# Kernel tuning notes

Measured on AMD Instinct MI355X. Metric: run time of the kernel, lower is better.

The kernel has to match this reference:

```python
import jax, jax.numpy as jnp
import numpy as np

B = 4096
HIST = 50
VOCAB = 100000
PAD_IDX = 179
EMB_DIM = 64           # sparse_dim_after_embedding
DENSE = 256            # dense_feature_number
PROJ_IN = 768          # emb_feature_dim_before_project
PROJ_HID = 256
PROJ_OUT = 64          # emb_feature_dim
BOT = (512, 64)        # bottom_mlp_dims
ALL_DIM = EMB_DIM + BOT[1] + PROJ_OUT        # 192
OUT_DIM = ALL_DIM * (ALL_DIM + 1) // 2 + BOT[1]  # 18592
TOP = (1024, 512)      # top_mlp_dims
BN_EPS = 1e-5

# precomputed upper-triangular (incl. diagonal) indices, row-major like torch mask extract
_TRIU_R, _TRIU_C = np.triu_indices(ALL_DIM)


def setup_inputs() -> dict:
    key = jax.random.key(0)
    ks = jax.random.split(key, 20)
    s = 0.02
    emb_table = jax.random.normal(ks[0], (VOCAB, EMB_DIM), jnp.float32) * s
    emb_table = emb_table.at[PAD_IDX].set(0.0)  # padding_idx=179
    return {
        "x_sparse": jax.random.randint(ks[1], (B, HIST), 0, VOCAB),
        "x_dense": jax.random.normal(ks[2], (B, DENSE), jnp.float32),
        "x_embed_before_projection": jax.random.normal(ks[3], (B, PROJ_IN), jnp.float32),
        "emb_table": emb_table,
        "pw1": jax.random.normal(ks[4], (PROJ_IN, PROJ_HID), jnp.float32) * s,
        "pb1": jnp.zeros((PROJ_HID,), jnp.float32),
        "pw2": jax.random.normal(ks[5], (PROJ_HID, PROJ_OUT), jnp.float32) * s,
        "pb2": jnp.zeros((PROJ_OUT,), jnp.float32),
        "bn_gamma": jnp.ones((PROJ_OUT,), jnp.float32),
        "bn_beta": jnp.zeros((PROJ_OUT,), jnp.float32),
        "bw1": jax.random.normal(ks[6], (DENSE, BOT[0]), jnp.float32) * s,
        "bb1": jnp.zeros((BOT[0],), jnp.float32),
        "bw2": jax.random.normal(ks[7], (BOT[0], BOT[1]), jnp.float32) * s,
        "bb2": jnp.zeros((BOT[1],), jnp.float32),
        "tw1": jax.random.normal(ks[8], (OUT_DIM, TOP[0]), jnp.float32) * s,
        "tb1": jnp.zeros((TOP[0],), jnp.float32),
        "tw2": jax.random.normal(ks[9], (TOP[0], TOP[1]), jnp.float32) * s,
        "tb2": jnp.zeros((TOP[1],), jnp.float32),
        "tw3": jax.random.normal(ks[10], (TOP[1], 1), jnp.float32) * s,
        "tb3": jnp.zeros((1,), jnp.float32),
    }


def reference(x_sparse, x_dense, x_embed_before_projection, emb_table,
              pw1, pb1, pw2, pb2, bn_gamma, bn_beta,
              bw1, bb1, bw2, bb2, tw1, tb1, tw2, tb2, tw3, tb3):
    # embedding-sum over history: [B, HIST, EMB_DIM] -> [B, EMB_DIM]
    embed_x = jnp.sum(emb_table[x_sparse], axis=1)

    # ContrastiveNet: Linear -> ReLU -> Linear -> BatchNorm1d (batch stats, training fwd)
    h = jax.nn.relu(x_embed_before_projection @ pw1 + pb1)
    z = h @ pw2 + pb2
    mu = jnp.mean(z, axis=0)
    var = jnp.var(z, axis=0)  # biased variance, as torch BN uses for normalization
    x_embed = bn_gamma * (z - mu) * jax.lax.rsqrt(var + BN_EPS) + bn_beta

    # bottom MLP (dropout = identity at inference)
    bottom = jax.nn.relu(jax.nn.relu(x_dense @ bw1 + bb1) @ bw2 + bb2)

    concat_first = jnp.concatenate([bottom, x_embed, embed_x], axis=-1)  # [B, 192]

    # pairwise dot-product interaction; pack upper triangle incl. diagonal
    dot = jnp.einsum('bi,bj->bij', concat_first, concat_first)  # [B, 192, 192]
    interaction = dot[:, _TRIU_R, _TRIU_C]  # [B, 192*193/2]

    concat_second = jnp.concatenate([interaction, bottom], axis=-1)  # [B, OUT_DIM]

    t = jax.nn.relu(concat_second @ tw1 + tb1)
    t = jax.nn.relu(t @ tw2 + tb2)
    output = jax.nn.sigmoid(t @ tw3 + tb3)  # [B, 1]
    # squeeze(-1).squeeze().unsqueeze(1) -> [B, 1]
    output = output.reshape(-1, 1)
    return output, x_embed
```

## Files before the change

kernel.cpp:

```cpp
#include <hip/hip_runtime.h>
#include <hip/hip_bf16.h>
#include <cstdint>
#include <cstddef>

typedef __bf16 bf16;
typedef unsigned char u8;
typedef unsigned short u16;
typedef __bf16 v8bf  __attribute__((ext_vector_type(8)));
typedef float  f32x4 __attribute__((ext_vector_type(4)));
typedef float  f32x16 __attribute__((ext_vector_type(16)));
typedef int    i32x4 __attribute__((ext_vector_type(4)));
typedef int    v8i32 __attribute__((ext_vector_type(8)));

__device__ __forceinline__ void async16(void* lds, const void* g) {
  __builtin_amdgcn_global_load_lds(
      (const __attribute__((address_space(1))) unsigned int*)g,
      (__attribute__((address_space(3))) unsigned int*)lds, 16, 0, 0);
}



__device__ __forceinline__ void pairs_dev(u16* __restrict__ pairs) {
  int r = threadIdx.x;
  if (r < 192) {
    int off = 192 * r - (r * (r - 1)) / 2;
    for (int c = r; c < 192; ++c) pairs[off + c - r] = (u16)((r << 8) | c);
  } else if (r == 192) {
    for (int j = 0; j < 64; ++j) pairs[18528 + j] = (u16)((j << 8) | 192);
  } else if (r == 193) {
    for (int j = 18592; j < 18624; ++j) pairs[j] = (u16)((192 << 8) | 192);
  }
}

__device__ __forceinline__ void packA_dev(const float* __restrict__ A,
                                          bf16* __restrict__ Ap, int K,
                                          int bx, int by) {
  const int t = threadIdx.x;
  const int KT = K >> 5;
  const size_t tile = ((size_t)bx * KT + by) * (64 * 32);
  const int c = t;
  const int mm = c >> 2, koct = (c & 3) * 8;
  const float* src = A + (size_t)(bx * 64 + mm) * K + by * 32 + koct;
  f32x4 f0 = *(const f32x4*)src;
  f32x4 f1 = *(const f32x4*)(src + 4);
  __align__(16) bf16 h[8];
  h[0]=(bf16)f0[0]; h[1]=(bf16)f0[1]; h[2]=(bf16)f0[2]; h[3]=(bf16)f0[3];
  h[4]=(bf16)f1[0]; h[5]=(bf16)f1[1]; h[6]=(bf16)f1[2]; h[7]=(bf16)f1[3];
  *(i32x4*)(Ap + tile + (size_t)c * 8) = *(const i32x4*)h;
}

__device__ __forceinline__ void packB_dev(const float* __restrict__ B,
                                          bf16* __restrict__ Bp, int K, int N,
                                          int bx, int by,
                                          float* __restrict__ sLB) {
  const int BNp = 64, LS = 66;
  const int t = threadIdx.x;
  const int KT = K >> 5;
  for (int idx = t; idx < 32 * BNp; idx += 256) {
    const int kk = idx >> 6, nn = idx & 63;
    sLB[kk * LS + nn] = B[(size_t)(by * 32 + kk) * N + bx * BNp + nn];
  }
  __syncthreads();
  const size_t tile = ((size_t)bx * KT + by) * ((size_t)BNp * 32);
  for (int c = t; c < BNp * 4; c += 256) {
    const int nn = c >> 2, koct = (c & 3) * 8;
    __align__(16) bf16 h[8];
#pragma unroll
    for (int j = 0; j < 8; ++j) h[j] = (bf16)sLB[(koct + j) * LS + nn];
    *(i32x4*)(Bp + tile + (size_t)c * 8) = *(const i32x4*)h;
  }
}

__device__ __forceinline__ void packTw1_dev(const float* __restrict__ tw1,
                                            u8* __restrict__ Bp, int nt, int kw,
                                            float* __restrict__ sLB) {
  const int t = threadIdx.x;
  u8* tile = Bp + ((size_t)nt * 291 + kw) * 8192;
#pragma unroll
  for (int ph = 0; ph < 2; ++ph) {
    if (ph) __syncthreads();
#pragma unroll
    for (int idx = t; idx < 1024; idx += 256) {
      const int kk = idx >> 5, nn4 = (idx & 31) * 4;
      const int gk = kw * 64 + ph * 32 + kk;
      f32x4 v = f32x4{0.f, 0.f, 0.f, 0.f};
      if (gk < 18592) {
        v = *(const f32x4*)(tw1 + (size_t)gk * 1024 + nt * 128 + nn4);
        v *= 32.f;
      }
      *(f32x4*)(sLB + kk * 132 + nn4) = v;
    }
    __syncthreads();
    const int nn = t >> 1;
    const int hkb = (t & 1) * 16;
    const int c = nn * 4 + ph * 2 + (t & 1);
    i32x4 d;
#pragma unroll
    for (int g = 0; g < 4; ++g) {
      const float p0 = sLB[(hkb + g * 4 + 0) * 132 + nn];
      const float p1 = sLB[(hkb + g * 4 + 1) * 132 + nn];
      const float p2 = sLB[(hkb + g * 4 + 2) * 132 + nn];
      const float p3 = sLB[(hkb + g * 4 + 3) * 132 + nn];
      int r = __builtin_amdgcn_cvt_pk_fp8_f32(p0, p1, 0, false);
      r = __builtin_amdgcn_cvt_pk_fp8_f32(p2, p3, r, true);
      d[g] = r;
    }
    *(i32x4*)(tile + c * 16) = d;
  }
}

__global__ __launch_bounds__(256) void prologue_kernel(
    const float* __restrict__ xep, const float* __restrict__ xd,
    const float* __restrict__ pw1, const float* __restrict__ pw2,
    const float* __restrict__ bw1, const float* __restrict__ bw2,
    const float* __restrict__ tw1, const float* __restrict__ tw2,
    bf16* Xp, bf16* Xd, bf16* Bpw1, bf16* Bpw2, bf16* Bbw1, bf16* Bbw2,
    u8* Btw1, bf16* Btw2, u16* pairs) {
  __shared__ float sLB[32 * 132];
  int i = blockIdx.x;
  if (i < 2328) { packTw1_dev(tw1, Btw1, i & 7, i >> 3, sLB); return; }
  i -= 2328;
  if (i < 1536) { packA_dev(xep, Xp, 768, i & 63, i >> 6); return; }
  i -= 1536;
  if (i < 512)  { packA_dev(xd, Xd, 256, i & 63, i >> 6); return; }
  i -= 512;
  if (i < 96)   { packB_dev(pw1, Bpw1, 768, 256, i & 3, i >> 2, sLB); return; }
  i -= 96;
  if (i < 8)    { packB_dev(pw2, Bpw2, 256, 64, 0, i, sLB); return; }
  i -= 8;
  if (i < 64)   { packB_dev(bw1, Bbw1, 256, 512, i & 7, i >> 3, sLB); return; }
  i -= 64;
  if (i < 16)   { packB_dev(bw2, Bbw2, 512, 64, 0, i, sLB); return; }
  i -= 16;
  if (i < 256)  { packB_dev(tw2, Btw2, 1024, 512, i & 7, i >> 3, sLB); return; }
  i -= 256;
  if (i == 0) pairs_dev(pairs);
}

__device__ __forceinline__ void embed8_dev(const int* __restrict__ xs,
                                           const float* __restrict__ emb,
                                           float* __restrict__ cf, int blk) {
  const int wid = threadIdx.x >> 6, lane = threadIdx.x & 63;
#pragma unroll
  for (int s = 0; s < 2; ++s) {
    const int b = blk * 8 + s * 4 + wid;
    const int* row = xs + (size_t)b * 50;
    float acc = 0.f;
    for (int h = 0; h < 50; ++h) {
      int idx = row[h];
      acc += emb[(size_t)idx * 64 + lane];
    }
    cf[(size_t)b * 193 + 128 + lane] = acc;
  }
}

template <int BM, int BN, int MF, int NF>
__device__ __forceinline__ void gemm_body(
    const bf16* __restrict__ Ap, const bf16* __restrict__ Bp,
    const float* __restrict__ bias,
    float* __restrict__ outF, int ldF,
    bf16* __restrict__ outP, int ktN, int bmsh,
    int KT, int M0, int relu_flag, int bx, int by,
    bf16* sA, bf16* sB) {
  const int t = threadIdx.x;
  const int wid = t >> 6, lane = t & 63;
  const int wm = (wid >> 1) * (MF * 16);
  const int wn = (wid & 1) * (NF * 16);
  const int r16 = lane & 15, q = lane >> 4;

  f32x4 acc[MF][NF];
#pragma unroll
  for (int i = 0; i < MF; ++i)
#pragma unroll
    for (int j = 0; j < NF; ++j) acc[i][j] = f32x4{0.f, 0.f, 0.f, 0.f};

  const bf16* aBase = Ap + (size_t)bx * KT * (BM * 32);
  const bf16* bBase = Bp + (size_t)by * KT * (BN * 32);
  constexpr int A_CH = BM * 4;
  constexpr int B_CH = BN * 4;

  for (int kt = 0; kt < KT; ++kt) {
    const bf16* ag = aBase + (size_t)kt * (BM * 32);
    const bf16* bg = bBase + (size_t)kt * (BN * 32);
#pragma unroll
    for (int c = t; c < A_CH; c += 256) {
      const int row = c >> 2, qs = c & 3, qg = (qs - (row >> 1)) & 3;
      async16(sA + c * 8, ag + row * 32 + qg * 8);
    }
#pragma unroll
    for (int c = t; c < B_CH; c += 256) {
      const int row = c >> 2, qs = c & 3, qg = (qs - (row >> 1)) & 3;
      async16(sB + c * 8, bg + row * 32 + qg * 8);
    }
    __syncthreads();
    v8bf af[MF], bfr[NF];
#pragma unroll
    for (int i = 0; i < MF; ++i) {
      const int row = wm + i * 16 + r16;
      af[i] = *(const v8bf*)(sA + row * 32 + (((q + (row >> 1)) & 3) * 8));
    }
#pragma unroll
    for (int j = 0; j < NF; ++j) {
      const int row = wn + j * 16 + r16;
      bfr[j] = *(const v8bf*)(sB + row * 32 + (((q + (row >> 1)) & 3) * 8));
    }
#pragma unroll
    for (int i = 0; i < MF; ++i)
#pragma unroll
      for (int j = 0; j < NF; ++j)
        acc[i][j] = __builtin_amdgcn_mfma_f32_16x16x32_bf16(af[i], bfr[j], acc[i][j], 0, 0, 0);
    __syncthreads();
  }

#pragma unroll
  for (int j = 0; j < NF; ++j) {
    const int gn = by * BN + wn + j * 16 + r16;
    const float bv = bias[gn];
#pragma unroll
    for (int i = 0; i < MF; ++i) {
      const int gm0 = M0 + bx * BM + wm + i * 16 + q * 4;
#pragma unroll
      for (int r = 0; r < 4; ++r) {
        float v = acc[i][j][r] + bv;
        if (relu_flag) v = fmaxf(v, 0.f);
        const int gm = gm0 + r;
        if (outF) outF[(size_t)gm * ldF + gn] = v;
        if (outP) {
          const int mt = gm >> bmsh, mm = gm & ((1 << bmsh) - 1);
          outP[(((size_t)mt * ktN + (gn >> 5)) << (bmsh + 5)) + ((size_t)mm << 5) + (gn & 31)] = (bf16)v;
        }
      }
    }
  }
}

template <int BM, int BN, int MF, int NF>
__global__ __launch_bounds__(256, 2) void gemm_kernel(
    const bf16* __restrict__ Ap, const bf16* __restrict__ Bp,
    const float* __restrict__ bias,
    float* __restrict__ outF, int ldF,
    bf16* __restrict__ outP, int ktN, int bmsh,
    int KT, int M0, int relu_flag) {
  __shared__ __align__(16) bf16 sA[BM * 32];
  __shared__ __align__(16) bf16 sB[BN * 32];
  gemm_body<BM, BN, MF, NF>(Ap, Bp, bias, outF, ldF, outP, ktN, bmsh,
                            KT, M0, relu_flag, blockIdx.x, blockIdx.y, sA, sB);
}

template <int BM, int BN, int MF, int NF>
__global__ __launch_bounds__(256, 2) void gemm_dual_kernel(
    const bf16* Ap0, const bf16* Bp0, const float* bias0,
    float* outF0, int ldF0, bf16* outP0, int ktN0, int bmsh0, int KT0, int relu0, int gy0,
    const bf16* Ap1, const bf16* Bp1, const float* bias1,
    float* outF1, int ldF1, bf16* outP1, int ktN1, int bmsh1, int KT1, int relu1, int gy1,
    const int* xs, const float* emb, float* cf) {
  __shared__ __align__(16) bf16 sA[BM * 32];
  __shared__ __align__(16) bf16 sB[BN * 32];
  if (blockIdx.z == 0) {
    if ((int)blockIdx.y >= gy0) return;
    gemm_body<BM, BN, MF, NF>(Ap0, Bp0, bias0, outF0, ldF0, outP0, ktN0, bmsh0,
                              KT0, 0, relu0, blockIdx.x, blockIdx.y, sA, sB);
  } else if (blockIdx.z == 1) {
    if ((int)blockIdx.y >= gy1) return;
    gemm_body<BM, BN, MF, NF>(Ap1, Bp1, bias1, outF1, ldF1, outP1, ktN1, bmsh1,
                              KT1, 0, relu1, blockIdx.x, blockIdx.y, sA, sB);
  } else {
    embed8_dev(xs, emb, cf, blockIdx.y * 64 + blockIdx.x);
  }
}

__global__ __launch_bounds__(256, 3) void gemm_splitk_mx(
    const u8* __restrict__ Ap, const u8* __restrict__ Bp,
    bf16* __restrict__ part, int S, int Mchunk) {
  __shared__ __align__(16) u8 sA[2][8192];
  __shared__ __align__(16) u8 sB[2][8192];
  const int t = threadIdx.x;
  const int bx = blockIdx.x, by = blockIdx.y, bz = blockIdx.z;
  const int wid = t >> 6, lane = t & 63;
  const int wm = (wid >> 1) * 64, wn = (wid & 1) * 64;
  const int l31 = lane & 31, khalf = lane >> 5;
  const int kw0 = (291 * bz) / S, kw1 = (291 * (bz + 1)) / S;

  f32x16 acc[2][2];
#pragma unroll
  for (int i = 0; i < 2; ++i)
#pragma unroll
    for (int j = 0; j < 2; ++j)
#pragma unroll
      for (int r = 0; r < 16; ++r) acc[i][j][r] = 0.f;

  const u8* aBase = Ap + (size_t)bx * 291 * 8192;
  const u8* bBase = Bp + (size_t)by * 291 * 8192;

  auto stage = [&](int buf, int kw) {
    const u8* ag = aBase + (size_t)kw * 8192;
    const u8* bg = bBase + (size_t)kw * 8192;
#pragma unroll
    for (int c = t; c < 512; c += 256) {
      const int row = c >> 2, qs = c & 3, qg = (qs - (row >> 1)) & 3;
      async16(sA[buf] + c * 16, ag + row * 64 + qg * 16);
    }
#pragma unroll
    for (int c = t; c < 512; c += 256) {
      const int row = c >> 2, qs = c & 3, qg = (qs - (row >> 1)) & 3;
      async16(sB[buf] + c * 16, bg + row * 64 + qg * 16);
    }
  };
  auto frag = [&](const u8* s, int row) -> v8i32 {
    const int q0 = (khalf * 2 + (row >> 1)) & 3;
    const int q1 = (khalf * 2 + 1 + (row >> 1)) & 3;
    union { i32x4 h[2]; v8i32 v; } u;
    u.h[0] = *(const i32x4*)(s + row * 64 + q0 * 16);
    u.h[1] = *(const i32x4*)(s + row * 64 + q1 * 16);
    return u.v;
  };
  auto compute = [&](int buf) {
    v8i32 av[2], bv[2];
#pragma unroll
    for (int i = 0; i < 2; ++i) av[i] = frag(sA[buf], wm + i * 32 + l31);
#pragma unroll
    for (int j = 0; j < 2; ++j) bv[j] = frag(sB[buf], wn + j * 32 + l31);
#pragma unroll
    for (int i = 0; i < 2; ++i)
#pragma unroll
      for (int j = 0; j < 2; ++j)
        acc[i][j] = __builtin_amdgcn_mfma_scale_f32_32x32x64_f8f6f4(
            av[i], bv[j], acc[i][j], 0, 0,
            0, 0x7F7F7F7F,
            0, 0x7A7A7A7A);
  };

  int kw = kw0;
  for (; kw + 1 < kw1; kw += 2) {
    stage(0, kw);
    stage(1, kw + 1);
    __syncthreads();
    compute(0);
    compute(1);
    __syncthreads();
  }
  if (kw < kw1) {
    stage(0, kw);
    __syncthreads();
    compute(0);
    __syncthreads();
  }

  bf16* pBase = part + (size_t)bz * Mchunk * 1024;
#pragma unroll
  for (int i = 0; i < 2; ++i)
#pragma unroll
    for (int j = 0; j < 2; ++j) {
      const int gn = by * 128 + wn + j * 32 + l31;
#pragma unroll
      for (int r = 0; r < 16; ++r) {
        const int gm = bx * 128 + wm + i * 32 + (r & 3) + 8 * (r >> 2) + 4 * khalf;
        pBase[(size_t)gm * 1024 + gn] = (bf16)acc[i][j][r];
      }
    }
}

__global__ __launch_bounds__(256) void reducek_kernel(const bf16* __restrict__ part,
                                                      const float* __restrict__ bias,
                                                      bf16* __restrict__ t1,
                                                      int S, int Mchunk, int M0) {
  const int idx = blockIdx.x * 256 + threadIdx.x;
  const int gm = idx >> 7;
  const int gn8 = (idx & 127) * 8;
  float v[8] = {0.f, 0.f, 0.f, 0.f, 0.f, 0.f, 0.f, 0.f};
  for (int s = 0; s < S; ++s) {
    v8bf p = *(const v8bf*)(part + ((size_t)s * Mchunk + gm) * 1024 + gn8);
#pragma unroll
    for (int r = 0; r < 8; ++r) v[r] += (float)p[r];
  }
  const f32x4 b0 = *(const f32x4*)(bias + gn8);
  const f32x4 b1 = *(const f32x4*)(bias + gn8 + 4);
  __align__(16) bf16 h[8];
#pragma unroll
  for (int r = 0; r < 4; ++r) h[r] = (bf16)fmaxf(v[r] + b0[r], 0.f);
#pragma unroll
  for (int r = 0; r < 4; ++r) h[4 + r] = (bf16)fmaxf(v[4 + r] + b1[r], 0.f);
  const int G = M0 + gm;
  const int mt = G >> 6, mm = G & 63, kt = gn8 >> 5;
  *(i32x4*)(t1 + (((size_t)mt * 32 + kt) << 11) + (mm << 5) + (gn8 & 31)) = *(const i32x4*)h;
}

__global__ __launch_bounds__(256) void bnstats_kernel(const float* __restrict__ z,
                                                      float* __restrict__ stats) {
  const int j = blockIdx.x, t = threadIdx.x;
  float s = 0.f, s2 = 0.f;
  for (int b = t; b < 4096; b += 256) {
    float v = z[(size_t)b * 64 + j];
    s += v; s2 += v * v;
  }
  __shared__ float sh[256], sh2[256];
  sh[t] = s; sh2[t] = s2;
  __syncthreads();
  for (int o = 128; o > 0; o >>= 1) {
    if (t < o) { sh[t] += sh[t + o]; sh2[t] += sh2[t + o]; }
    __syncthreads();
  }
  if (t == 0) {
    float mu = sh[0] * (1.f / 4096.f);
    float var = sh2[0] * (1.f / 4096.f) - mu * mu;
    stats[j] = mu;
    stats[64 + j] = rsqrtf(var + 1e-5f);
  }
}

__global__ __launch_bounds__(256) void cfbuild_kernel(const float* __restrict__ z,
                                                      const float* __restrict__ stats,
                                                      const float* __restrict__ gamma,
                                                      const float* __restrict__ beta,
                                                      float* __restrict__ cf,
                                                      float* __restrict__ dout) {
  const int wid = threadIdx.x >> 6, lane = threadIdx.x & 63;
  const int b = blockIdx.x * 4 + wid;
  const float mu = stats[lane], rstd = stats[64 + lane];
  const float xe = gamma[lane] * (z[(size_t)b * 64 + lane] - mu) * rstd + beta[lane];
  cf[(size_t)b * 193 + 64 + lane] = xe;
  dout[4096 + (size_t)b * 64 + lane] = xe;
  if (lane == 0) cf[(size_t)b * 193 + 192] = 1.f;
}

__global__ __launch_bounds__(256, 2) void agen_kernel(const float* __restrict__ cf,
                                                      const u16* __restrict__ pairs,
                                                      u8* __restrict__ Ap, int rowBase) {
  __shared__ float sCF[64 * 193];
  const int t = threadIdx.x;
  const int gRow0 = rowBase + blockIdx.x * 64;
  for (int i = t; i < 64 * 193; i += 256) sCF[i] = cf[(size_t)gRow0 * 193 + i];
  __syncthreads();
  const int kw0 = (291 * blockIdx.y) / 8;
  const int kw1 = (291 * (blockIdx.y + 1)) / 8;
  const int row = t >> 2, kq = t & 3;
  const int mt = blockIdx.x >> 1;
  const int mrow = (blockIdx.x & 1) * 64 + row;
  const float* myrow = sCF + row * 193;
  for (int kw = kw0; kw < kw1; ++kw) {
    const int kb = kw * 64 + kq * 16;
    union { i32x4 v4[2]; u16 u[16]; } P;
    P.v4[0] = *(const i32x4*)(pairs + kb);
    P.v4[1] = *(const i32x4*)(pairs + kb + 8);
    i32x4 d;
#pragma unroll
    for (int g = 0; g < 4; ++g) {
      float p[4];
#pragma unroll
      for (int j = 0; j < 4; ++j) {
        const u16 pr = P.u[g * 4 + j];
        p[j] = myrow[pr >> 8] * myrow[pr & 255];
      }
      int r = __builtin_amdgcn_cvt_pk_fp8_f32(p[0], p[1], 0, false);
      r = __builtin_amdgcn_cvt_pk_fp8_f32(p[2], p[3], r, true);
      d[g] = r;
    }
    *(i32x4*)(Ap + (((size_t)mt * 291 + kw) * 128 + mrow) * 64 + kq * 16) = d;
  }
}

__global__ __launch_bounds__(256) void topdot_kernel(const float* __restrict__ t2,
                                                     const float* __restrict__ w,
                                                     const float* __restrict__ b3,
                                                     float* __restrict__ dout) {
  const int wid = threadIdx.x >> 6, lane = threadIdx.x & 63;
  const int b = blockIdx.x * 4 + wid;
  const f32x4* row = (const f32x4*)(t2 + (size_t)b * 512);
  const f32x4* wv = (const f32x4*)w;
  float s = 0.f;
#pragma unroll
  for (int i = 0; i < 2; ++i) {
    f32x4 a = row[lane * 2 + i], c = wv[lane * 2 + i];
    s += a[0] * c[0] + a[1] * c[1] + a[2] * c[2] + a[3] * c[3];
  }
  for (int m = 32; m > 0; m >>= 1) s += __shfl_xor(s, m, 64);
  if (lane == 0) dout[b] = 1.f / (1.f + __expf(-(s + b3[0])));
}

extern "C" void kernel_launch(void* const* d_in, const int* in_sizes, int n_in,
                              void* d_out, int out_size, void* d_ws, size_t ws_size,
                              hipStream_t stream) {
  const int*   xs   = (const int*)  d_in[0];
  const float* xd   = (const float*)d_in[1];
  const float* xep  = (const float*)d_in[2];
  const float* emb  = (const float*)d_in[3];
  const float* pw1  = (const float*)d_in[4];
  const float* pb1  = (const float*)d_in[5];
  const float* pw2  = (const float*)d_in[6];
  const float* pb2  = (const float*)d_in[7];
  const float* gmma = (const float*)d_in[8];
  const float* beta = (const float*)d_in[9];
  const float* bw1  = (const float*)d_in[10];
  const float* bb1  = (const float*)d_in[11];
  const float* bw2  = (const float*)d_in[12];
  const float* bb2  = (const float*)d_in[13];
  const float* tw1  = (const float*)d_in[14];
  const float* tb1  = (const float*)d_in[15];
  const float* tw2  = (const float*)d_in[16];
  const float* tb2  = (const float*)d_in[17];
  const float* tw3  = (const float*)d_in[18];
  const float* tb3  = (const float*)d_in[19];
  float* out = (float*)d_out;

  uint8_t* base = (uint8_t*)d_ws;
  size_t off = 0;
  auto alloc = [&](size_t b) {
    void* p = base + off;
    off = (off + b + 511) & ~((size_t)511);
    return p;
  };
  u16*  pairs = (u16*) alloc((size_t)18624 * 2);
  bf16* Xp    = (bf16*)alloc((size_t)4096 * 768 * 2);
  bf16* Xd    = (bf16*)alloc((size_t)4096 * 256 * 2);
  bf16* Bpw1  = (bf16*)alloc((size_t)768 * 256 * 2);
  bf16* Bpw2  = (bf16*)alloc((size_t)256 * 64 * 2);
  bf16* Bbw1  = (bf16*)alloc((size_t)256 * 512 * 2);
  bf16* Bbw2  = (bf16*)alloc((size_t)512 * 64 * 2);
  u8*   Btw1  = (u8*)  alloc((size_t)8 * 291 * 8192);
  bf16* Btw2  = (bf16*)alloc((size_t)1024 * 512 * 2);
  bf16* hbuf  = (bf16*)alloc((size_t)4096 * 256 * 2);
  float* z    = (float*)alloc((size_t)4096 * 64 * 4);
  float* stats= (float*)alloc((size_t)128 * 4);
  bf16* b0    = (bf16*)alloc((size_t)4096 * 512 * 2);
  float* cf   = (float*)alloc((size_t)4096 * 193 * 4);
  bf16* t1    = (bf16*)alloc((size_t)4096 * 1024 * 2);
  float* t2   = (float*)alloc((size_t)4096 * 512 * 4);
  size_t fixedEnd = off;

  int chunk = 512, S = 8;
  {
    const int candC[5] = {4096, 4096, 2048, 1024, 512};
    const int candS[5] = {8, 4, 8, 8, 8};
    for (int i = 0; i < 5; ++i) {
      size_t need = fixedEnd + (size_t)candC[i] * 18624 + 1024 +
                    (size_t)candS[i] * candC[i] * 1024 * 2 + 1024;
      if (need <= ws_size) { chunk = candC[i]; S = candS[i]; break; }
    }
  }
  u8*   ApBig = (u8*)  alloc((size_t)chunk * 18624);
  bf16* partK = (bf16*)alloc((size_t)S * chunk * 1024 * 2);

  prologue_kernel<<<4817, 256, 0, stream>>>(
      xep, xd, pw1, pw2, bw1, bw2, tw1, tw2,
      Xp, Xd, Bpw1, Bpw2, Bbw1, Bbw2, Btw1, Btw2, pairs);

  gemm_dual_kernel<64, 64, 2, 2><<<dim3(64, 8, 3), 256, 0, stream>>>(
      Xp, Bpw1, pb1, nullptr, 0, hbuf, 8, 6, 24, 1, 4,
      Xd, Bbw1, bb1, nullptr, 0, b0, 16, 6, 8, 1, 8,
      xs, emb, cf);
  gemm_dual_kernel<64, 64, 2, 2><<<dim3(64, 1, 2), 256, 0, stream>>>(
      hbuf, Bpw2, pb2, z, 64, nullptr, 0, 0, 8, 0, 1,
      b0, Bbw2, bb2, cf, 193, nullptr, 0, 0, 16, 1, 1,
      nullptr, nullptr, nullptr);

  bnstats_kernel<<<64, 256, 0, stream>>>(z, stats);
  cfbuild_kernel<<<1024, 256, 0, stream>>>(z, stats, gmma, beta, cf, out);

  for (int c0 = 0; c0 < 4096; c0 += chunk) {
    agen_kernel<<<dim3(chunk / 64, 8), 256, 0, stream>>>(cf, pairs, ApBig, c0);
    gemm_splitk_mx<<<dim3(chunk / 128, 8, S), 256, 0, stream>>>(
        ApBig, Btw1, partK, S, chunk);
    reducek_kernel<<<chunk / 2, 256, 0, stream>>>(partK, tb1, t1, S, chunk, c0);
  }

  gemm_kernel<64, 64, 2, 2><<<dim3(64, 8), 256, 0, stream>>>(
      t1, Btw2, tb2, t2, 512, nullptr, 0, 0, 32, 0, 1);
  topdot_kernel<<<1024, 256, 0, stream>>>(t2, tw3, tb3, out);
}
```

Before: 360.6 us.

## Fuse BN normalize into agen, retune split-K and streamline FP8 GEMM staging

Removes the cfbuild kernel by computing the batch-norm output inside agen_kernel while it loads the feature rows into shared memory, and writes x_embed from the y==0 blocks. The split-K FP8 GEMM is templated on S, raises its launch bound to four blocks per SM, and precomputes its LDS and global offsets for the async loads and fragment reads. The workspace candidates now prefer S=4 at full chunk size, the embedding loop is unrolled, and agen skips pair products for padded K. The trade-offs are fewer split-K blocks to fill the GPU and possible register pressure from the occupancy bound.

```diff
diff --git a/kernel.cpp b/kernel.cpp
--- a/kernel.cpp
+++ b/kernel.cpp
@@ -17,7 +17,6 @@
       (const __attribute__((address_space(1))) unsigned int*)g,
       (__attribute__((address_space(3))) unsigned int*)lds, 16, 0, 0);
 }
-
 
 
 __device__ __forceinline__ void pairs_dev(u16* __restrict__ pairs) {
@@ -146,6 +145,7 @@
     const int b = blk * 8 + s * 4 + wid;
     const int* row = xs + (size_t)b * 50;
     float acc = 0.f;
+#pragma unroll 10
     for (int h = 0; h < 50; ++h) {
       int idx = row[h];
       acc += emb[(size_t)idx * 64 + lane];
@@ -269,18 +269,38 @@
   }
 }
 
-__global__ __launch_bounds__(256, 3) void gemm_splitk_mx(
+template <int S>
+__global__ __launch_bounds__(256, 4) void gemm_splitk_mx(
     const u8* __restrict__ Ap, const u8* __restrict__ Bp,
-    bf16* __restrict__ part, int S, int Mchunk) {
-  __shared__ __align__(16) u8 sA[2][8192];
-  __shared__ __align__(16) u8 sB[2][8192];
+    bf16* __restrict__ part, int Mchunk) {
+  __shared__ __align__(16) u8 sAB[4][8192];
   const int t = threadIdx.x;
   const int bx = blockIdx.x, by = blockIdx.y, bz = blockIdx.z;
-  const int wid = t >> 6, lane = t & 63;
+  const int lane = t & 63, wid = t >> 6;
   const int wm = (wid >> 1) * 64, wn = (wid & 1) * 64;
   const int l31 = lane & 31, khalf = lane >> 5;
   const int kw0 = (291 * bz) / S, kw1 = (291 * (bz + 1)) / S;
 
+  const int r1 = t >> 2;
+  const int g1 = r1 * 64 + ((((t & 3) - (r1 >> 1)) & 3) << 4);
+  const int r2 = (t + 256) >> 2;
+  const int g2 = r2 * 64 + (((((t + 256) & 3) - (r2 >> 1)) & 3) << 4);
+  u8* lA = &sAB[0][0] + t * 16;
+  u8* lB = &sAB[2][0] + t * 16;
+
+  const u8* fa0[2]; const u8* fa1[2]; const u8* fb0[2]; const u8* fb1[2];
+#pragma unroll
+  for (int i = 0; i < 2; ++i) {
+    const int ra = wm + i * 32 + l31;
+    const int qa = (khalf * 2 + (ra >> 1)) & 3;
+    fa0[i] = &sAB[0][0] + ra * 64 + qa * 16;
+    fa1[i] = &sAB[0][0] + ra * 64 + (((qa + 1) & 3) << 4);
+    const int rb = wn + i * 32 + l31;
+    const int qb = (khalf * 2 + (rb >> 1)) & 3;
+    fb0[i] = &sAB[2][0] + rb * 64 + qb * 16;
+    fb1[i] = &sAB[2][0] + rb * 64 + (((qb + 1) & 3) << 4);
+  }
+
   f32x16 acc[2][2];
 #pragma unroll
   for (int i = 0; i < 2; ++i)
@@ -289,37 +309,22 @@
 #pragma unroll
       for (int r = 0; r < 16; ++r) acc[i][j][r] = 0.f;
 
-  const u8* aBase = Ap + (size_t)bx * 291 * 8192;
-  const u8* bBase = Bp + (size_t)by * 291 * 8192;
-
-  auto stage = [&](int buf, int kw) {
-    const u8* ag = aBase + (size_t)kw * 8192;
-    const u8* bg = bBase + (size_t)kw * 8192;
-#pragma unroll
-    for (int c = t; c < 512; c += 256) {
-      const int row = c >> 2, qs = c & 3, qg = (qs - (row >> 1)) & 3;
-      async16(sA[buf] + c * 16, ag + row * 64 + qg * 16);
-    }
-#pragma unroll
-    for (int c = t; c < 512; c += 256) {
-      const int row = c >> 2, qs = c & 3, qg = (qs - (row >> 1)) & 3;
-      async16(sB[buf] + c * 16, bg + row * 64 + qg * 16);
-    }
-  };
-  auto frag = [&](const u8* s, int row) -> v8i32 {
-    const int q0 = (khalf * 2 + (row >> 1)) & 3;
-    const int q1 = (khalf * 2 + 1 + (row >> 1)) & 3;
-    union { i32x4 h[2]; v8i32 v; } u;
-    u.h[0] = *(const i32x4*)(s + row * 64 + q0 * 16);
-    u.h[1] = *(const i32x4*)(s + row * 64 + q1 * 16);
-    return u.v;
-  };
-  auto compute = [&](int buf) {
+  const u8* agp = Ap + ((size_t)bx * 291 + kw0) * 8192;
+  const u8* bgp = Bp + ((size_t)by * 291 + kw0) * 8192;
+
+  auto compute = [&](int off) {
     v8i32 av[2], bv[2];
 #pragma unroll
-    for (int i = 0; i < 2; ++i) av[i] = frag(sA[buf], wm + i * 32 + l31);
-#pragma unroll
-    for (int j = 0; j < 2; ++j) bv[j] = frag(sB[buf], wn + j * 32 + l31);
+    for (int i = 0; i < 2; ++i) {
+      union { i32x4 h[2]; v8i32 v; } ua;
+      ua.h[0] = *(const i32x4*)(fa0[i] + off);
+      ua.h[1] = *(const i32x4*)(fa1[i] + off);
+      av[i] = ua.v;
+      union { i32x4 h[2]; v8i32 v; } ub;
+      ub.h[0] = *(const i32x4*)(fb0[i] + off);
+      ub.h[1] = *(const i32x4*)(fb1[i] + off);
+      bv[i] = ub.v;
+    }
 #pragma unroll
     for (int i = 0; i < 2; ++i)
 #pragma unroll
@@ -330,17 +335,22 @@
             0, 0x7A7A7A7A);
   };
 
-  int kw = kw0;
-  for (; kw + 1 < kw1; kw += 2) {
-    stage(0, kw);
-    stage(1, kw + 1);
+  const int nw = kw1 - kw0;
+  int w = 0;
+  for (; w + 2 <= nw; w += 2) {
+    async16(lA, agp + g1);         async16(lA + 4096, agp + g2);
+    async16(lB, bgp + g1);         async16(lB + 4096, bgp + g2);
+    async16(lA + 8192, agp + 8192 + g1); async16(lA + 12288, agp + 8192 + g2);
+    async16(lB + 8192, bgp + 8192 + g1); async16(lB + 12288, bgp + 8192 + g2);
+    agp += 16384; bgp += 16384;
     __syncthreads();
     compute(0);
-    compute(1);
-    __syncthreads();
-  }
-  if (kw < kw1) {
-    stage(0, kw);
+    compute(8192);
+    __syncthreads();
+  }
+  if (w < nw) {
+    async16(lA, agp + g1); async16(lA + 4096, agp + g2);
+    async16(lB, bgp + g1); async16(lB + 4096, bgp + g2);
     __syncthreads();
     compute(0);
     __syncthreads();
@@ -408,29 +418,35 @@
   }
 }
 
-__global__ __launch_bounds__(256) void cfbuild_kernel(const float* __restrict__ z,
+__global__ __launch_bounds__(256, 2) void agen_kernel(const float* __restrict__ cf,
+                                                      const float* __restrict__ z,
                                                       const float* __restrict__ stats,
                                                       const float* __restrict__ gamma,
                                                       const float* __restrict__ beta,
-                                                      float* __restrict__ cf,
-                                                      float* __restrict__ dout) {
-  const int wid = threadIdx.x >> 6, lane = threadIdx.x & 63;
-  const int b = blockIdx.x * 4 + wid;
-  const float mu = stats[lane], rstd = stats[64 + lane];
-  const float xe = gamma[lane] * (z[(size_t)b * 64 + lane] - mu) * rstd + beta[lane];
-  cf[(size_t)b * 193 + 64 + lane] = xe;
-  dout[4096 + (size_t)b * 64 + lane] = xe;
-  if (lane == 0) cf[(size_t)b * 193 + 192] = 1.f;
-}
-
-__global__ __launch_bounds__(256, 2) void agen_kernel(const float* __restrict__ cf,
                                                       const u16* __restrict__ pairs,
-                                                      u8* __restrict__ Ap, int rowBase) {
+                                                      u8* __restrict__ Ap,
+                                                      float* __restrict__ dout,
+                                                      int rowBase) {
   __shared__ float sCF[64 * 193];
   const int t = threadIdx.x;
   const int gRow0 = rowBase + blockIdx.x * 64;
-  for (int i = t; i < 64 * 193; i += 256) sCF[i] = cf[(size_t)gRow0 * 193 + i];
+  for (int idx = t; idx < 64 * 64; idx += 256) {
+    const int r = idx >> 6, c = idx & 63;
+    sCF[r * 193 + c] = cf[(size_t)(gRow0 + r) * 193 + c];
+  }
+  for (int idx = t; idx < 64 * 64; idx += 256) {
+    const int r = idx >> 6, c = idx & 63;
+    sCF[r * 193 + 128 + c] = cf[(size_t)(gRow0 + r) * 193 + 128 + c];
+  }
+  for (int idx = t; idx < 64 * 64; idx += 256) {
+    const int r = idx >> 6, c = idx & 63;
+    const float xe = gamma[c] * (z[(size_t)(gRow0 + r) * 64 + c] - stats[c]) * stats[64 + c] + beta[c];
+    sCF[r * 193 + 64 + c] = xe;
+    if (blockIdx.y == 0) dout[4096 + (size_t)(gRow0 + r) * 64 + c] = xe;
+  }
+  if (t < 64) sCF[t * 193 + 192] = 1.f;
   __syncthreads();
+
   const int kw0 = (291 * blockIdx.y) / 8;
   const int kw1 = (291 * (blockIdx.y + 1)) / 8;
   const int row = t >> 2, kq = t & 3;
@@ -439,21 +455,25 @@
   const float* myrow = sCF + row * 193;
   for (int kw = kw0; kw < kw1; ++kw) {
     const int kb = kw * 64 + kq * 16;
-    union { i32x4 v4[2]; u16 u[16]; } P;
-    P.v4[0] = *(const i32x4*)(pairs + kb);
-    P.v4[1] = *(const i32x4*)(pairs + kb + 8);
     i32x4 d;
-#pragma unroll
-    for (int g = 0; g < 4; ++g) {
-      float p[4];
-#pragma unroll
-      for (int j = 0; j < 4; ++j) {
-        const u16 pr = P.u[g * 4 + j];
-        p[j] = myrow[pr >> 8] * myrow[pr & 255];
+    if (kb >= 18592) {
+      d = i32x4{0, 0, 0, 0};
+    } else {
+      union { i32x4 v4[2]; u16 u[16]; } P;
+      P.v4[0] = *(const i32x4*)(pairs + kb);
+      P.v4[1] = *(const i32x4*)(pairs + kb + 8);
+#pragma unroll
+      for (int g = 0; g < 4; ++g) {
+        float p[4];
+#pragma unroll
+        for (int j = 0; j < 4; ++j) {
+          const u16 pr = P.u[g * 4 + j];
+          p[j] = myrow[pr >> 8] * myrow[pr & 255];
+        }
+        int r = __builtin_amdgcn_cvt_pk_fp8_f32(p[0], p[1], 0, false);
+        r = __builtin_amdgcn_cvt_pk_fp8_f32(p[2], p[3], r, true);
+        d[g] = r;
       }
-      int r = __builtin_amdgcn_cvt_pk_fp8_f32(p[0], p[1], 0, false);
-      r = __builtin_amdgcn_cvt_pk_fp8_f32(p[2], p[3], r, true);
-      d[g] = r;
     }
     *(i32x4*)(Ap + (((size_t)mt * 291 + kw) * 128 + mrow) * 64 + kq * 16) = d;
   }
@@ -529,8 +549,8 @@
 
   int chunk = 512, S = 8;
   {
-    const int candC[5] = {4096, 4096, 2048, 1024, 512};
-    const int candS[5] = {8, 4, 8, 8, 8};
+    const int candC[5] = {4096, 2048, 2048, 1024, 512};
+    const int candS[5] = {4, 8, 4, 8, 8};
     for (int i = 0; i < 5; ++i) {
       size_t need = fixedEnd + (size_t)candC[i] * 18624 + 1024 +
                     (size_t)candS[i] * candC[i] * 1024 * 2 + 1024;
@@ -554,12 +574,16 @@
       nullptr, nullptr, nullptr);
 
   bnstats_kernel<<<64, 256, 0, stream>>>(z, stats);
-  cfbuild_kernel<<<1024, 256, 0, stream>>>(z, stats, gmma, beta, cf, out);
 
   for (int c0 = 0; c0 < 4096; c0 += chunk) {
-    agen_kernel<<<dim3(chunk / 64, 8), 256, 0, stream>>>(cf, pairs, ApBig, c0);
-    gemm_splitk_mx<<<dim3(chunk / 128, 8, S), 256, 0, stream>>>(
-        ApBig, Btw1, partK, S, chunk);
+    agen_kernel<<<dim3(chunk / 64, 8), 256, 0, stream>>>(
+        cf, z, stats, gmma, beta, pairs, ApBig, out, c0);
+    if (S == 4)
+      gemm_splitk_mx<4><<<dim3(chunk / 128, 8, 4), 256, 0, stream>>>(
+          ApBig, Btw1, partK, chunk);
+    else
+      gemm_splitk_mx<8><<<dim3(chunk / 128, 8, 8), 256, 0, stream>>>(
+          ApBig, Btw1, partK, chunk);
     reducek_kernel<<<chunk / 2, 256, 0, stream>>>(partK, tb1, t1, S, chunk, c0);
   }
 
```

After: 353.6 us. No clear change (-1.9%).
